# Performance work log

Hardware: AMD Instinct MI355X
Metric: run time of the kernel (lower is better)

Reference implementation:

```python
import jax, jax.numpy as jnp
import numpy as np

ROI = 7
NMS_THR = 0.01
NMS_SIZE = 100


def crop_and_resize(fmap, boxes, crop):
    # fmap [H,W,C], boxes [N,4] normalized (y1,x1,y2,x2) -> [N,crop,crop,C]
    H, W, C = fmap.shape
    t = jnp.linspace(0.0, 1.0, crop)
    ys = (boxes[:, 0:1] + (boxes[:, 2:3] - boxes[:, 0:1]) * t) * (H - 1)  # [N,crop]
    xs = (boxes[:, 1:2] + (boxes[:, 3:4] - boxes[:, 1:2]) * t) * (W - 1)
    y0 = jnp.clip(jnp.floor(ys), 0, H - 1).astype(jnp.int32)
    x0 = jnp.clip(jnp.floor(xs), 0, W - 1).astype(jnp.int32)
    y1 = jnp.clip(y0 + 1, 0, H - 1)
    x1 = jnp.clip(x0 + 1, 0, W - 1)
    wy = (ys - y0)[:, :, None, None]
    wx = (xs - x0)[:, None, :, None]
    Y0, Y1 = y0[:, :, None], y1[:, :, None]
    X0, X1 = x0[:, None, :], x1[:, None, :]
    f00 = fmap[Y0, X0]; f01 = fmap[Y0, X1]
    f10 = fmap[Y1, X0]; f11 = fmap[Y1, X1]
    return (f00 * (1 - wy) * (1 - wx) + f01 * (1 - wy) * wx
            + f10 * wy * (1 - wx) + f11 * wy * wx)


def iou_matrix(b):
    # b [N,4] (x1,y1,x2,y2)
    area = jnp.maximum(b[:, 2] - b[:, 0], 0) * jnp.maximum(b[:, 3] - b[:, 1], 0)
    lt = jnp.maximum(b[:, None, :2], b[None, :, :2])
    rb = jnp.minimum(b[:, None, 2:], b[None, :, 2:])
    wh = jnp.maximum(rb - lt, 0.0)
    inter = wh[..., 0] * wh[..., 1]
    return inter / (area[:, None] + area[None, :] - inter + 1e-8)


def nms(boxes, scores, thr, max_out):
    # greedy NMS, fixed-size output (pads with lowest-ranked boxes when fewer survive)
    N = boxes.shape[0]
    order = jnp.argsort(-scores)
    M = iou_matrix(boxes[order])
    idx = jnp.arange(N)
    def body(i, keep):
        sup = (M[i] > thr) & (idx > i) & keep[i]
        return keep & ~sup
    keep = jax.lax.fori_loop(0, N, body, jnp.ones(N, dtype=bool))
    rank = jnp.where(keep, idx, N + idx)
    sel = jnp.argsort(rank)[:max_out]
    return order[sel]


def make_boxes(key, n):
    kc, ks = jax.random.split(key)
    c = jax.random.uniform(kc, (n, 2), minval=0.1, maxval=0.9)
    s = jax.random.uniform(ks, (n, 2), minval=0.02, maxval=0.15)
    lo = jnp.clip(c - s / 2, 0.0, 1.0)
    hi = jnp.clip(c + s / 2, 0.0, 1.0)
    return jnp.concatenate([lo, hi], axis=1)  # (y1,x1,y2,x2)


def setup_inputs() -> dict:
    key = jax.random.key(0)
    ks = jax.random.split(key, 12)
    N, D, Hd = 1024, ROI * ROI * 32, 2048
    img_boxes = make_boxes(ks[0], N)
    bev_boxes = make_boxes(ks[1], N)
    bev_boxes_abs = bev_boxes[:, jnp.array([1, 0, 3, 2])] * 80.0  # (x1,y1,x2,y2) in meters
    def w(k, shape, fan_in):
        return jax.random.normal(k, shape, jnp.float32) * (2.0 / fan_in) ** 0.5
    return {
        'img_feat_map': jax.random.uniform(ks[2], (1, 360, 1200, 32), jnp.float32),
        'bev_feat_map': jax.random.uniform(ks[3], (1, 700, 800, 32), jnp.float32),
        'img_boxes': img_boxes,
        'bev_boxes': bev_boxes,
        'bev_boxes_abs': bev_boxes_abs,
        'img_mask': jnp.ones((1, 1, 1, 1), jnp.float32),
        'bev_mask': jnp.ones((1, 1, 1, 1), jnp.float32),
        'W1': w(ks[4], (D, Hd), D), 'b1': jnp.zeros((Hd,), jnp.float32),
        'W2': w(ks[5], (Hd, Hd), Hd), 'b2': jnp.zeros((Hd,), jnp.float32),
        'Wc': w(ks[6], (Hd, 2), Hd), 'bc': jnp.zeros((2,), jnp.float32),
        'Wo': w(ks[7], (Hd, 10), Hd), 'bo': jnp.zeros((10,), jnp.float32),
        'Wa': w(ks[8], (Hd, 2), Hd), 'ba': jnp.zeros((2,), jnp.float32),
    }


def reference(img_feat_map, bev_feat_map, img_boxes, bev_boxes, bev_boxes_abs,
              img_mask, bev_mask, W1, b1, W2, b2, Wc, bc, Wo, bo, Wa, ba):
    # ROI align on masked feature maps
    rois_rgb = crop_and_resize((img_mask * img_feat_map)[0], img_boxes, ROI)
    rois_bev = crop_and_resize((bev_mask * bev_feat_map)[0], bev_boxes, ROI)
    # mean fusion
    fused = (rois_rgb + rois_bev) / (img_mask + bev_mask)  # [N,7,7,32]
    # predictor
    x = fused.reshape(fused.shape[0], -1)
    h = jax.nn.relu(x @ W1 + b1)
    h = jax.nn.relu(h @ W2 + b2)
    obj = h @ Wc + bc            # [N,2]
    off = h @ Wo + bo            # [N,10]
    ang = h @ Wa + ba            # [N,2]
    obj_soft = jax.nn.softmax(obj, axis=1)
    orient = jnp.arctan2(ang[:, 1], ang[:, 0])  # convert_angle_to_orientation
    # offset-adjusted BEV boxes for NMS
    pb = bev_boxes_abs + 0.1 * off[:, :4]
    boxes = jnp.stack([jnp.minimum(pb[:, 0], pb[:, 2]), jnp.minimum(pb[:, 1], pb[:, 3]),
                       jnp.maximum(pb[:, 0], pb[:, 2]), jnp.maximum(pb[:, 1], pb[:, 3])], axis=1)
    scores = jnp.max(obj[:, 1:], axis=1)
    ti = nms(jax.lax.stop_gradient(boxes), jax.lax.stop_gradient(scores), NMS_THR, NMS_SIZE)
    # [100, 2 + 4 + 1]: softmax scores, pred bev boxes, orientations
    return jnp.concatenate([obj_soft[ti], boxes[ti], orient[ti][:, None]], axis=1)
```

## Files before the change

kernel.cpp:

```cpp
#include <hip/hip_runtime.h>
#include <math.h>

#define NBOX 1024
#define ROI_N 7
#define CH 32
#define FEAT (ROI_N*ROI_N*CH)
#define K1PAD 1664
#define HD 2048
#define NMS_THR_F 0.01f
#define NMS_OUT 100
#define MTRI_WORDS 8704

typedef _Float16 f16;
typedef f16 f16x4 __attribute__((ext_vector_type(4)));
typedef f16 f16x8 __attribute__((ext_vector_type(8)));
typedef float f32x4 __attribute__((ext_vector_type(4)));

__device__ __forceinline__ void split_f16(float v, f16& h, f16& l) {
  h = (f16)v;
  l = (f16)((v - (float)h) * 4096.0f);
}

__device__ __forceinline__ void gload_lds16(const void* g, void* l) {
  __builtin_amdgcn_global_load_lds(
      (const __attribute__((address_space(1))) unsigned int*)g,
      (__attribute__((address_space(3))) unsigned int*)l, 16, 0, 0);
}

#define B_ROI 1024
#define B_C1  (64*26)
#define B_C2  (64*32)
#define B_INIT 2048

__device__ void roi_part(int b, int tid,
    const float* __restrict__ img, const float* __restrict__ bev,
    const float* __restrict__ img_boxes, const float* __restrict__ bev_boxes,
    float mi, float mb, f16* __restrict__ xh, f16* __restrict__ xl)
{
  const float denom = mi + mb;
  if (tid >= 196) {
    const int g = tid - 196;
    if (g < 12) {
      f16x8 z = {};
      *(f16x8*)&xh[(size_t)b*K1PAD + FEAT + g*8] = z;
      *(f16x8*)&xl[(size_t)b*K1PAD + FEAT + g*8] = z;
    }
    return;
  }
  const int cell = tid >> 2, cg = (tid & 3) * 8;
  const int ti = cell / ROI_N, tj = cell - ti*ROI_N;
  const float tt_i = (ti == 6) ? 1.0f : ti * (1.0f/6.0f);
  const float tt_j = (tj == 6) ? 1.0f : tj * (1.0f/6.0f);

  float vi[8], vb[8];
  {
    const int H = 360, W = 1200;
    const float iy0 = img_boxes[b*4+0], ix0 = img_boxes[b*4+1];
    const float iy1 = img_boxes[b*4+2], ix1 = img_boxes[b*4+3];
    const float ys = (iy0 + (iy1 - iy0) * tt_i) * (float)(H-1);
    const float xs = (ix0 + (ix1 - ix0) * tt_j) * (float)(W-1);
    int y0 = (int)floorf(ys); y0 = y0 < 0 ? 0 : (y0 > H-1 ? H-1 : y0);
    int x0 = (int)floorf(xs); x0 = x0 < 0 ? 0 : (x0 > W-1 ? W-1 : x0);
    const int y1 = (y0+1 > H-1) ? H-1 : y0+1;
    const int x1 = (x0+1 > W-1) ? W-1 : x0+1;
    const float wy = ys - (float)y0, wx = xs - (float)x0;
    const float w00 = (1.0f-wy)*(1.0f-wx), w01 = (1.0f-wy)*wx;
    const float w10 = wy*(1.0f-wx),        w11 = wy*wx;
    const float* p00 = &img[(y0*W + x0)*CH + cg];
    const float* p01 = &img[(y0*W + x1)*CH + cg];
    const float* p10 = &img[(y1*W + x0)*CH + cg];
    const float* p11 = &img[(y1*W + x1)*CH + cg];
#pragma unroll
    for (int q = 0; q < 2; ++q) {
      const float4 f00 = *(const float4*)(p00 + q*4);
      const float4 f01 = *(const float4*)(p01 + q*4);
      const float4 f10 = *(const float4*)(p10 + q*4);
      const float4 f11 = *(const float4*)(p11 + q*4);
      vi[q*4+0] = f00.x*w00 + f01.x*w01 + f10.x*w10 + f11.x*w11;
      vi[q*4+1] = f00.y*w00 + f01.y*w01 + f10.y*w10 + f11.y*w11;
      vi[q*4+2] = f00.z*w00 + f01.z*w01 + f10.z*w10 + f11.z*w11;
      vi[q*4+3] = f00.w*w00 + f01.w*w01 + f10.w*w10 + f11.w*w11;
    }
  }
  {
    const int H = 700, W = 800;
    const float by0 = bev_boxes[b*4+0], bx0 = bev_boxes[b*4+1];
    const float by1 = bev_boxes[b*4+2], bx1 = bev_boxes[b*4+3];
    const float ys = (by0 + (by1 - by0) * tt_i) * (float)(H-1);
    const float xs = (bx0 + (bx1 - bx0) * tt_j) * (float)(W-1);
    int y0 = (int)floorf(ys); y0 = y0 < 0 ? 0 : (y0 > H-1 ? H-1 : y0);
    int x0 = (int)floorf(xs); x0 = x0 < 0 ? 0 : (x0 > W-1 ? W-1 : x0);
    const int y1 = (y0+1 > H-1) ? H-1 : y0+1;
    const int x1 = (x0+1 > W-1) ? W-1 : x0+1;
    const float wy = ys - (float)y0, wx = xs - (float)x0;
    const float w00 = (1.0f-wy)*(1.0f-wx), w01 = (1.0f-wy)*wx;
    const float w10 = wy*(1.0f-wx),        w11 = wy*wx;
    const float* p00 = &bev[(y0*W + x0)*CH + cg];
    const float* p01 = &bev[(y0*W + x1)*CH + cg];
    const float* p10 = &bev[(y1*W + x0)*CH + cg];
    const float* p11 = &bev[(y1*W + x1)*CH + cg];
#pragma unroll
    for (int q = 0; q < 2; ++q) {
      const float4 f00 = *(const float4*)(p00 + q*4);
      const float4 f01 = *(const float4*)(p01 + q*4);
      const float4 f10 = *(const float4*)(p10 + q*4);
      const float4 f11 = *(const float4*)(p11 + q*4);
      vb[q*4+0] = f00.x*w00 + f01.x*w01 + f10.x*w10 + f11.x*w11;
      vb[q*4+1] = f00.y*w00 + f01.y*w01 + f10.y*w10 + f11.y*w11;
      vb[q*4+2] = f00.z*w00 + f01.z*w01 + f10.z*w10 + f11.z*w11;
      vb[q*4+3] = f00.w*w00 + f01.w*w01 + f10.w*w10 + f11.w*w11;
    }
  }
  f16x8 h8, l8;
#pragma unroll
  for (int q = 0; q < 8; ++q) {
    f16 h, l;
    split_f16((mi*vi[q] + mb*vb[q]) / denom, h, l);
    h8[q] = h; l8[q] = l;
  }
  const size_t o = (size_t)b*K1PAD + cell*32 + cg;
  *(f16x8*)&xh[o] = h8;
  *(f16x8*)&xl[o] = l8;
}

__global__ __launch_bounds__(256) void prep_kernel(
    const float* __restrict__ img, const float* __restrict__ bev,
    const float* __restrict__ img_boxes, const float* __restrict__ bev_boxes,
    const float* __restrict__ img_mask, const float* __restrict__ bev_mask,
    f16* __restrict__ xh, f16* __restrict__ xl,
    const float* __restrict__ W1, f16* __restrict__ Wt1h, f16* __restrict__ Wt1l,
    const float* __restrict__ W2, f16* __restrict__ Wt2h, f16* __restrict__ Wt2l,
    const float* __restrict__ b1, const float* __restrict__ b2,
    float4* __restrict__ h1f, float4* __restrict__ h2f)
{
  __shared__ float t[64][33];
  const int g = blockIdx.x;
  const int tid = threadIdx.x;

  if (g < B_ROI) {
    roi_part(g, tid, img, bev, img_boxes, bev_boxes, img_mask[0], bev_mask[0], xh, xl);
    return;
  }
  const float* W; f16 *Wh, *Wl; int K, Kpad, cb;
  if (g < B_ROI + B_C1) { cb = g - B_ROI;        W = W1; Wh = Wt1h; Wl = Wt1l; K = FEAT; Kpad = K1PAD; }
  else if (g < B_ROI + B_C1 + B_C2) { cb = g - B_ROI - B_C1; W = W2; Wh = Wt2h; Wl = Wt2l; K = HD; Kpad = HD; }
  else {
    const int ib = g - B_ROI - B_C1 - B_C2;
    const int idx = ib*256 + tid;
    const int c4 = idx & (HD/4 - 1);
    h1f[idx] = *(const float4*)&b1[c4*4];
    h2f[idx] = *(const float4*)&b2[c4*4];
    return;
  }
  const int nt = cb & 63, kt = cb >> 6;
  const int n0 = nt * 32, k0 = kt * 64;
#pragma unroll
  for (int p = 0; p < 8; ++p) {
    const int idx = tid + p*256;
    const int kk = idx >> 5, nn = idx & 31;
    const int k = k0 + kk;
    t[kk][nn] = (k < K) ? W[(size_t)k*HD + n0 + nn] : 0.0f;
  }
  __syncthreads();
  const int nn = tid >> 3;
  const int kg = (tid & 7) * 8;
  f16x8 h8, l8;
#pragma unroll
  for (int q = 0; q < 8; ++q) {
    f16 h, l;
    split_f16(t[kg + q][nn], h, l);
    h8[q] = h; l8[q] = l;
  }
  *(f16x8*)&Wh[(size_t)(n0+nn)*Kpad + k0 + kg] = h8;
  *(f16x8*)&Wl[(size_t)(n0+nn)*Kpad + k0 + kg] = l8;
}

__global__ __launch_bounds__(256) void split_relu_kernel(
    const float* __restrict__ in, f16* __restrict__ oh, f16* __restrict__ ol)
{
  const int idx = blockIdx.x*256 + threadIdx.x;
  const float4 v = *(const float4*)&in[idx*4];
  f16x4 h4, l4;
  { f16 h,l; split_f16(fmaxf(v.x,0.0f),h,l); h4[0]=h; l4[0]=l; }
  { f16 h,l; split_f16(fmaxf(v.y,0.0f),h,l); h4[1]=h; l4[1]=l; }
  { f16 h,l; split_f16(fmaxf(v.z,0.0f),h,l); h4[2]=h; l4[2]=l; }
  { f16 h,l; split_f16(fmaxf(v.w,0.0f),h,l); h4[3]=h; l4[3]=l; }
  *(f16x4*)&oh[idx*4] = h4;
  *(f16x4*)&ol[idx*4] = l4;
}

__global__ __launch_bounds__(256, 2) void gemm_sk(
    const f16* __restrict__ Ah_g, const f16* __restrict__ Al_g,
    const f16* __restrict__ Bh_g, const f16* __restrict__ Bl_g,
    float* __restrict__ Cout, int M, int N, int K, int kchunk)
{
  __shared__ __align__(16) f16 Ah[128][32], Al[128][32], Bh[128][32], Bl[128][32];
  const int tid = threadIdx.x;

  const int g = blockIdx.x;
  const int xcd = g & 7, c = g >> 3;
  const int nb = xcd*2 + (c & 1);
  const int mb = (c >> 1) & 7;
  const int zb = c >> 4;
  const int m0 = mb * 128, n0 = nb * 128;
  const int kb = zb * kchunk, ke = kb + kchunk;

  const int wid = tid >> 6, lane = tid & 63;
  const int wr = wid >> 1, wc = wid & 1;
  const int frow = lane & 15, fkg = lane >> 4;
  const int swz = (fkg ^ ((frow >> 1) & 3)) * 8;

  const f16* sarr; f16* larr; int rbase;
  if (wid == 0)      { sarr = Ah_g; larr = &Ah[0][0]; rbase = m0; }
  else if (wid == 1) { sarr = Al_g; larr = &Al[0][0]; rbase = m0; }
  else if (wid == 2) { sarr = Bh_g; larr = &Bh[0][0]; rbase = n0; }
  else               { sarr = Bl_g; larr = &Bl[0][0]; rbase = n0; }
  const int lr = lane >> 2, lg = lane & 3;

  f32x4 acc1[4][4], acc2[4][4];
#pragma unroll
  for (int i = 0; i < 4; ++i)
#pragma unroll
    for (int j = 0; j < 4; ++j)
#pragma unroll
      for (int r = 0; r < 4; ++r) { acc1[i][j][r] = 0.0f; acc2[i][j][r] = 0.0f; }

  for (int kk = kb; kk < ke; kk += 32) {
    __syncthreads();
#pragma unroll
    for (int q = 0; q < 8; ++q) {
      const int r = q*16 + lr;
      const int sg = lg ^ ((r >> 1) & 3);
      gload_lds16(&sarr[(size_t)(rbase + r)*K + kk + sg*8], larr + q*512);
    }
    __syncthreads();

    f16x8 bh[4], bl[4];
#pragma unroll
    for (int j = 0; j < 4; ++j) {
      const int rr = wc*64 + j*16 + frow;
      bh[j] = *(const f16x8*)&Bh[rr][swz];
      bl[j] = *(const f16x8*)&Bl[rr][swz];
    }
#pragma unroll
    for (int i = 0; i < 4; ++i) {
      const int rr = wr*64 + i*16 + frow;
      const f16x8 ah = *(const f16x8*)&Ah[rr][swz];
      const f16x8 al = *(const f16x8*)&Al[rr][swz];
#pragma unroll
      for (int j = 0; j < 4; ++j) {
        acc1[i][j] = __builtin_amdgcn_mfma_f32_16x16x32_f16(ah, bh[j], acc1[i][j], 0, 0, 0);
        acc2[i][j] = __builtin_amdgcn_mfma_f32_16x16x32_f16(ah, bl[j], acc2[i][j], 0, 0, 0);
        acc2[i][j] = __builtin_amdgcn_mfma_f32_16x16x32_f16(al, bh[j], acc2[i][j], 0, 0, 0);
      }
    }
  }

  const float s = 1.0f / 4096.0f;
#pragma unroll
  for (int i = 0; i < 4; ++i)
#pragma unroll
    for (int j = 0; j < 4; ++j) {
      const int col = n0 + wc*64 + j*16 + frow;
#pragma unroll
      for (int r = 0; r < 4; ++r) {
        const int row = m0 + wr*64 + i*16 + fkg*4 + r;
        atomicAdd(&Cout[(size_t)row*N + col], acc1[i][j][r] + acc2[i][j][r] * s);
      }
    }
}

__global__ __launch_bounds__(256) void heads_kernel(
    const float* __restrict__ h2f,
    const float* __restrict__ Wc, const float* __restrict__ bc,
    const float* __restrict__ Wo, const float* __restrict__ bo,
    const float* __restrict__ Wa, const float* __restrict__ ba,
    const float* __restrict__ bev_abs,
    float* __restrict__ obj_soft, float* __restrict__ boxes,
    float* __restrict__ orient, float* __restrict__ scores)
{
  const int r = blockIdx.x;
  const int tid = threadIdx.x;
  float acc[14];
#pragma unroll
  for (int j = 0; j < 14; ++j) acc[j] = 0.0f;
  for (int k = tid; k < HD; k += 256) {
    const float hv = fmaxf(h2f[(size_t)r*HD + k], 0.0f);
    acc[0]  += hv * Wc[k*2+0];
    acc[1]  += hv * Wc[k*2+1];
#pragma unroll
    for (int j = 0; j < 10; ++j) acc[2+j] += hv * Wo[k*10+j];
    acc[12] += hv * Wa[k*2+0];
    acc[13] += hv * Wa[k*2+1];
  }
  __shared__ float red[14][256];
#pragma unroll
  for (int j = 0; j < 14; ++j) red[j][tid] = acc[j];
  __syncthreads();
  for (int s = 128; s > 0; s >>= 1) {
    if (tid < s) {
#pragma unroll
      for (int j = 0; j < 14; ++j) red[j][tid] += red[j][tid + s];
    }
    __syncthreads();
  }
  if (tid == 0) {
    const float obj0 = red[0][0] + bc[0];
    const float obj1 = red[1][0] + bc[1];
    float off0 = red[2][0] + bo[0];
    float off1 = red[3][0] + bo[1];
    float off2 = red[4][0] + bo[2];
    float off3 = red[5][0] + bo[3];
    const float a0 = red[12][0] + ba[0];
    const float a1 = red[13][0] + ba[1];

    const float m  = fmaxf(obj0, obj1);
    const float e0 = expf(obj0 - m), e1 = expf(obj1 - m);
    const float se = e0 + e1;
    obj_soft[r*2+0] = e0 / se;
    obj_soft[r*2+1] = e1 / se;
    orient[r] = atan2f(a1, a0);

    const float pb0 = bev_abs[r*4+0] + 0.1f*off0;
    const float pb1 = bev_abs[r*4+1] + 0.1f*off1;
    const float pb2 = bev_abs[r*4+2] + 0.1f*off2;
    const float pb3 = bev_abs[r*4+3] + 0.1f*off3;
    boxes[r*4+0] = fminf(pb0, pb2);
    boxes[r*4+1] = fminf(pb1, pb3);
    boxes[r*4+2] = fmaxf(pb0, pb2);
    boxes[r*4+3] = fmaxf(pb1, pb3);
    scores[r] = obj1;
  }
}

__global__ __launch_bounds__(128) void sort_kernel(
    const float* __restrict__ scores, const float* __restrict__ boxes,
    int* __restrict__ order, float4* __restrict__ sboxes, float* __restrict__ sarea)
{
  const int i = blockIdx.x * 128 + threadIdx.x;
  const float my = scores[i];
  int pos = 0;
  for (int j = 0; j < NBOX; ++j) {
    const float sj = scores[j];
    pos += (sj > my) || (sj == my && j < i);
  }
  const float b0 = boxes[i*4+0], b1 = boxes[i*4+1];
  const float b2 = boxes[i*4+2], b3 = boxes[i*4+3];
  order[pos]  = i;
  sboxes[pos] = make_float4(b0, b1, b2, b3);
  sarea[pos]  = fmaxf(b2 - b0, 0.0f) * fmaxf(b3 - b1, 0.0f);
}

__device__ __forceinline__ int tri_base(int i) {
  const int b = i >> 6;
  return 64*(16*b - (b*(b-1))/2) + (i & 63)*(16 - b);
}

__global__ __launch_bounds__(256) void maskbuild_kernel(
    const float4* __restrict__ sboxes, const float* __restrict__ sarea,
    unsigned long long* __restrict__ Mtri)
{
  __shared__ float4 sb[NBOX];
  __shared__ float  sa[NBOX];
  const int tid = threadIdx.x;
  for (int t = tid; t < NBOX; t += 256) { sb[t] = sboxes[t]; sa[t] = sarea[t]; }
  __syncthreads();
  const int wv = tid >> 6, lane = tid & 63;
  for (int r = 0; r < 4; ++r) {
    const int i = blockIdx.x * 16 + wv * 4 + r;
    const float4 bi = sb[i];
    const float  ai = sa[i];
    const int b = i >> 6;
    const int base = tri_base(i);
    for (int w = b; w < 16; ++w) {
      const int j = w * 64 + lane;
      const float4 bj = sb[j];
      const float lt0 = fmaxf(bi.x, bj.x), lt1 = fmaxf(bi.y, bj.y);
      const float rb0 = fminf(bi.z, bj.z), rb1 = fminf(bi.w, bj.w);
      const float wq = fmaxf(rb0 - lt0, 0.0f), hq = fmaxf(rb1 - lt1, 0.0f);
      const float inter = wq * hq;
      const float iou = inter / (ai + sa[j] - inter + 1e-8f);
      const unsigned long long bits = __ballot((j > i) && (iou > NMS_THR_F));
      if (lane == 0) Mtri[base + (w - b)] = bits;
    }
  }
}

__global__ __launch_bounds__(1024) void scan_out_kernel(
    const unsigned long long* __restrict__ Mtri_g, const int* __restrict__ order,
    const float4* __restrict__ sboxes, const float* __restrict__ obj_soft,
    const float* __restrict__ orient, float* __restrict__ out)
{
  __shared__ unsigned long long M[MTRI_WORDS];
  __shared__ unsigned long long keepw[16];
  const int tid = threadIdx.x;
  for (int t = tid; t < MTRI_WORDS; t += 1024) M[t] = Mtri_g[t];
  __syncthreads();

  if (tid < 64) {
    const int lane = tid;
    unsigned long long kw = (lane < 16) ? ~0ull : 0ull;
    for (int w = 0; w < 16; ++w) {
      unsigned long long rem = __shfl(kw, w);
      while (rem) {
        const int bpos = __builtin_ctzll(rem);
        const int i = w * 64 + bpos;
        const int base = tri_base(i);
        unsigned long long m = 0;
        if (lane >= w && lane < 16) m = M[base + (lane - w)];
        kw &= ~m;
        const unsigned long long updated = __shfl(kw, w);
        rem = (bpos == 63) ? 0ull : (updated & (~0ull << (bpos + 1)));
      }
    }
    if (lane < 16) keepw[lane] = kw;
  }
  __syncthreads();

  const int w = tid >> 6, bpos = tid & 63;
  int pre = 0, total = 0;
#pragma unroll
  for (int q = 0; q < 16; ++q) {
    const int pc = __popcll(keepw[q]);
    total += pc;
    if (q < w) pre += pc;
  }
  pre += __popcll(keepw[w] & ((bpos == 0) ? 0ull : (~0ull >> (64 - bpos))));
  const int keep_self = (int)((keepw[w] >> bpos) & 1ull);
  const int rank = keep_self ? pre : (total + tid - pre);

  if (rank < NMS_OUT) {
    const int ob = order[tid];
    const float4 bx = sboxes[tid];
    out[rank*7+0] = obj_soft[ob*2+0];
    out[rank*7+1] = obj_soft[ob*2+1];
    out[rank*7+2] = bx.x;
    out[rank*7+3] = bx.y;
    out[rank*7+4] = bx.z;
    out[rank*7+5] = bx.w;
    out[rank*7+6] = orient[ob];
  }
}

extern "C" void kernel_launch(void* const* d_in, const int* in_sizes, int n_in,
                              void* d_out, int out_size, void* d_ws, size_t ws_size,
                              hipStream_t stream) {
  (void)in_sizes; (void)n_in; (void)out_size; (void)ws_size;
  const float* img       = (const float*)d_in[0];
  const float* bev       = (const float*)d_in[1];
  const float* img_boxes = (const float*)d_in[2];
  const float* bev_boxes = (const float*)d_in[3];
  const float* bev_abs   = (const float*)d_in[4];
  const float* img_mask  = (const float*)d_in[5];
  const float* bev_mask  = (const float*)d_in[6];
  const float* W1 = (const float*)d_in[7];
  const float* b1 = (const float*)d_in[8];
  const float* W2 = (const float*)d_in[9];
  const float* b2 = (const float*)d_in[10];
  const float* Wc = (const float*)d_in[11];
  const float* bc = (const float*)d_in[12];
  const float* Wo = (const float*)d_in[13];
  const float* bo = (const float*)d_in[14];
  const float* Wa = (const float*)d_in[15];
  const float* ba = (const float*)d_in[16];
  float* out = (float*)d_out;

  char* ws = (char*)d_ws;
  f16* xh    = (f16*)ws;                                  ws += (size_t)NBOX*K1PAD*2;
  f16* xl    = (f16*)ws;                                  ws += (size_t)NBOX*K1PAD*2;
  float* h1f = (float*)ws;                                ws += (size_t)NBOX*HD*4;
  f16* h1h   = (f16*)ws;                                  ws += (size_t)NBOX*HD*2;
  f16* h1l   = (f16*)ws;                                  ws += (size_t)NBOX*HD*2;
  float* h2f = (float*)ws;                                ws += (size_t)NBOX*HD*4;
  f16* Wt1h  = (f16*)ws;                                  ws += (size_t)HD*K1PAD*2;
  f16* Wt1l  = (f16*)ws;                                  ws += (size_t)HD*K1PAD*2;
  f16* Wt2h  = (f16*)ws;                                  ws += (size_t)HD*HD*2;
  f16* Wt2l  = (f16*)ws;                                  ws += (size_t)HD*HD*2;
  float* obj_soft = (float*)ws;                           ws += NBOX*2*4;
  float* boxesf   = (float*)ws;                           ws += NBOX*4*4;
  float* orient   = (float*)ws;                           ws += NBOX*4;
  float* scores   = (float*)ws;                           ws += NBOX*4;
  int*   order    = (int*)ws;                             ws += NBOX*4;
  float4* sboxes  = (float4*)ws;                          ws += NBOX*16;
  float* sarea    = (float*)ws;                           ws += NBOX*4;
  unsigned long long* Mtri = (unsigned long long*)ws;

  prep_kernel<<<B_ROI + B_C1 + B_C2 + B_INIT, 256, 0, stream>>>(
      img, bev, img_boxes, bev_boxes, img_mask, bev_mask, xh, xl,
      W1, Wt1h, Wt1l, W2, Wt2h, Wt2l, b1, b2, (float4*)h1f, (float4*)h2f);
  gemm_sk<<<512, 256, 0, stream>>>(xh, xl, Wt1h, Wt1l, h1f, NBOX, HD, K1PAD, K1PAD/4);
  split_relu_kernel<<<NBOX*HD/4/256, 256, 0, stream>>>(h1f, h1h, h1l);
  gemm_sk<<<512, 256, 0, stream>>>(h1h, h1l, Wt2h, Wt2l, h2f, NBOX, HD, HD, HD/4);
  heads_kernel<<<NBOX, 256, 0, stream>>>(h2f, Wc, bc, Wo, bo, Wa, ba, bev_abs,
                                         obj_soft, boxesf, orient, scores);
  sort_kernel<<<8, 128, 0, stream>>>(scores, boxesf, order, sboxes, sarea);
  maskbuild_kernel<<<64, 256, 0, stream>>>(sboxes, sarea, Mtri);
  scan_out_kernel<<<1, 1024, 0, stream>>>(Mtri, order, sboxes, obj_soft, orient, out);
}
```

Before: 359.2 us.

## Double-buffer GEMM LDS staging, transpose head weights, cache scores in LDS

The split-K GEMM now uses two LDS buffers and issues the global-to-LDS loads for the next K step before computing on the current one, so there is one barrier per iteration instead of two. The head weights are concatenated and transposed into a contiguous [14][HD] array in the prep kernel, which lets the heads kernel read hidden values and weights as vectorized float4 loads. The sort kernel first copies the scores into shared memory. Doubling LDS use to 64KB per block may lower occupancy below the two blocks the launch bounds request.

Result: faster. 345.3 us (-3.9%).

```diff
diff --git a/kernel.cpp b/kernel.cpp
--- a/kernel.cpp
+++ b/kernel.cpp
@@ -31,6 +31,7 @@
 #define B_C1  (64*26)
 #define B_C2  (64*32)
 #define B_INIT 2048
+#define B_HT  112
 
 __device__ void roi_part(int b, int tid,
     const float* __restrict__ img, const float* __restrict__ bev,
@@ -131,7 +132,9 @@
     const float* __restrict__ W1, f16* __restrict__ Wt1h, f16* __restrict__ Wt1l,
     const float* __restrict__ W2, f16* __restrict__ Wt2h, f16* __restrict__ Wt2l,
     const float* __restrict__ b1, const float* __restrict__ b2,
-    float4* __restrict__ h1f, float4* __restrict__ h2f)
+    float4* __restrict__ h1f, float4* __restrict__ h2f,
+    const float* __restrict__ Wc, const float* __restrict__ Wo,
+    const float* __restrict__ Wa, float* __restrict__ Wcat)
 {
   __shared__ float t[64][33];
   const int g = blockIdx.x;
@@ -139,6 +142,16 @@
 
   if (g < B_ROI) {
     roi_part(g, tid, img, bev, img_boxes, bev_boxes, img_mask[0], bev_mask[0], xh, xl);
+    return;
+  }
+  if (g >= B_ROI + B_C1 + B_C2 + B_INIT) {
+    const int idx = (g - (B_ROI + B_C1 + B_C2 + B_INIT))*256 + tid;
+    const int j = idx >> 11, k = idx & (HD-1);
+    float v;
+    if (j < 2)       v = Wc[k*2 + j];
+    else if (j < 12) v = Wo[k*10 + (j-2)];
+    else             v = Wa[k*2 + (j-12)];
+    Wcat[idx] = v;
     return;
   }
   const float* W; f16 *Wh, *Wl; int K, Kpad, cb;
@@ -189,12 +202,23 @@
   *(f16x4*)&ol[idx*4] = l4;
 }
 
+#define STAGE(BUF, KK)                                                        \
+  do {                                                                        \
+    _Pragma("unroll")                                                         \
+    for (int q_ = 0; q_ < 8; ++q_) {                                          \
+      const int r_ = q_*16 + lr;                                              \
+      const int sg_ = lg ^ ((r_ >> 1) & 3);                                   \
+      gload_lds16(&sarr[(size_t)(rbase + r_)*K + (KK) + sg_*8],               \
+                  lbase + (BUF)*16384 + q_*512);                              \
+    }                                                                         \
+  } while (0)
+
 __global__ __launch_bounds__(256, 2) void gemm_sk(
     const f16* __restrict__ Ah_g, const f16* __restrict__ Al_g,
     const f16* __restrict__ Bh_g, const f16* __restrict__ Bl_g,
     float* __restrict__ Cout, int M, int N, int K, int kchunk)
 {
-  __shared__ __align__(16) f16 Ah[128][32], Al[128][32], Bh[128][32], Bl[128][32];
+  __shared__ __align__(16) f16 lds[2][4][128*32];
   const int tid = threadIdx.x;
 
   const int g = blockIdx.x;
@@ -210,11 +234,12 @@
   const int frow = lane & 15, fkg = lane >> 4;
   const int swz = (fkg ^ ((frow >> 1) & 3)) * 8;
 
-  const f16* sarr; f16* larr; int rbase;
-  if (wid == 0)      { sarr = Ah_g; larr = &Ah[0][0]; rbase = m0; }
-  else if (wid == 1) { sarr = Al_g; larr = &Al[0][0]; rbase = m0; }
-  else if (wid == 2) { sarr = Bh_g; larr = &Bh[0][0]; rbase = n0; }
-  else               { sarr = Bl_g; larr = &Bl[0][0]; rbase = n0; }
+  const f16* sarr; int rbase;
+  if (wid == 0)      { sarr = Ah_g; rbase = m0; }
+  else if (wid == 1) { sarr = Al_g; rbase = m0; }
+  else if (wid == 2) { sarr = Bh_g; rbase = n0; }
+  else               { sarr = Bl_g; rbase = n0; }
+  f16* lbase = &lds[0][wid][0];
   const int lr = lane >> 2, lg = lane & 3;
 
   f32x4 acc1[4][4], acc2[4][4];
@@ -225,28 +250,25 @@
 #pragma unroll
       for (int r = 0; r < 4; ++r) { acc1[i][j][r] = 0.0f; acc2[i][j][r] = 0.0f; }
 
+  STAGE(0, kb);
+  __syncthreads();
+  int cur = 0;
   for (int kk = kb; kk < ke; kk += 32) {
-    __syncthreads();
-#pragma unroll
-    for (int q = 0; q < 8; ++q) {
-      const int r = q*16 + lr;
-      const int sg = lg ^ ((r >> 1) & 3);
-      gload_lds16(&sarr[(size_t)(rbase + r)*K + kk + sg*8], larr + q*512);
-    }
-    __syncthreads();
-
+    if (kk + 32 < ke) STAGE(cur ^ 1, kk + 32);
+
+    const f16* bc_ = &lds[cur][0][0];
     f16x8 bh[4], bl[4];
 #pragma unroll
     for (int j = 0; j < 4; ++j) {
       const int rr = wc*64 + j*16 + frow;
-      bh[j] = *(const f16x8*)&Bh[rr][swz];
-      bl[j] = *(const f16x8*)&Bl[rr][swz];
+      bh[j] = *(const f16x8*)(bc_ + 8192  + rr*32 + swz);
+      bl[j] = *(const f16x8*)(bc_ + 12288 + rr*32 + swz);
     }
 #pragma unroll
     for (int i = 0; i < 4; ++i) {
       const int rr = wr*64 + i*16 + frow;
-      const f16x8 ah = *(const f16x8*)&Ah[rr][swz];
-      const f16x8 al = *(const f16x8*)&Al[rr][swz];
+      const f16x8 ah = *(const f16x8*)(bc_ +        rr*32 + swz);
+      const f16x8 al = *(const f16x8*)(bc_ + 4096 + rr*32 + swz);
 #pragma unroll
       for (int j = 0; j < 4; ++j) {
         acc1[i][j] = __builtin_amdgcn_mfma_f32_16x16x32_f16(ah, bh[j], acc1[i][j], 0, 0, 0);
@@ -254,6 +276,8 @@
         acc2[i][j] = __builtin_amdgcn_mfma_f32_16x16x32_f16(al, bh[j], acc2[i][j], 0, 0, 0);
       }
     }
+    __syncthreads();
+    cur ^= 1;
   }
 
   const float s = 1.0f / 4096.0f;
@@ -271,27 +295,29 @@
 }
 
 __global__ __launch_bounds__(256) void heads_kernel(
-    const float* __restrict__ h2f,
-    const float* __restrict__ Wc, const float* __restrict__ bc,
-    const float* __restrict__ Wo, const float* __restrict__ bo,
-    const float* __restrict__ Wa, const float* __restrict__ ba,
-    const float* __restrict__ bev_abs,
+    const float* __restrict__ h2f, const float* __restrict__ Wcat,
+    const float* __restrict__ bc, const float* __restrict__ bo,
+    const float* __restrict__ ba, const float* __restrict__ bev_abs,
     float* __restrict__ obj_soft, float* __restrict__ boxes,
     float* __restrict__ orient, float* __restrict__ scores)
 {
   const int r = blockIdx.x;
   const int tid = threadIdx.x;
+  const int k0 = tid * 8;
+  float4 hv0 = *(const float4*)&h2f[(size_t)r*HD + k0];
+  float4 hv1 = *(const float4*)&h2f[(size_t)r*HD + k0 + 4];
+  hv0.x = fmaxf(hv0.x, 0.0f); hv0.y = fmaxf(hv0.y, 0.0f);
+  hv0.z = fmaxf(hv0.z, 0.0f); hv0.w = fmaxf(hv0.w, 0.0f);
+  hv1.x = fmaxf(hv1.x, 0.0f); hv1.y = fmaxf(hv1.y, 0.0f);
+  hv1.z = fmaxf(hv1.z, 0.0f); hv1.w = fmaxf(hv1.w, 0.0f);
+
   float acc[14];
 #pragma unroll
-  for (int j = 0; j < 14; ++j) acc[j] = 0.0f;
-  for (int k = tid; k < HD; k += 256) {
-    const float hv = fmaxf(h2f[(size_t)r*HD + k], 0.0f);
-    acc[0]  += hv * Wc[k*2+0];
-    acc[1]  += hv * Wc[k*2+1];
-#pragma unroll
-    for (int j = 0; j < 10; ++j) acc[2+j] += hv * Wo[k*10+j];
-    acc[12] += hv * Wa[k*2+0];
-    acc[13] += hv * Wa[k*2+1];
+  for (int j = 0; j < 14; ++j) {
+    const float4 w0 = *(const float4*)&Wcat[j*HD + k0];
+    const float4 w1 = *(const float4*)&Wcat[j*HD + k0 + 4];
+    acc[j] = hv0.x*w0.x + hv0.y*w0.y + hv0.z*w0.z + hv0.w*w0.w
+           + hv1.x*w1.x + hv1.y*w1.y + hv1.z*w1.z + hv1.w*w1.w;
   }
   __shared__ float red[14][256];
 #pragma unroll
@@ -307,10 +333,10 @@
   if (tid == 0) {
     const float obj0 = red[0][0] + bc[0];
     const float obj1 = red[1][0] + bc[1];
-    float off0 = red[2][0] + bo[0];
-    float off1 = red[3][0] + bo[1];
-    float off2 = red[4][0] + bo[2];
-    float off3 = red[5][0] + bo[3];
+    const float off0 = red[2][0] + bo[0];
+    const float off1 = red[3][0] + bo[1];
+    const float off2 = red[4][0] + bo[2];
+    const float off3 = red[5][0] + bo[3];
     const float a0 = red[12][0] + ba[0];
     const float a1 = red[13][0] + ba[1];
 
@@ -337,11 +363,15 @@
     const float* __restrict__ scores, const float* __restrict__ boxes,
     int* __restrict__ order, float4* __restrict__ sboxes, float* __restrict__ sarea)
 {
-  const int i = blockIdx.x * 128 + threadIdx.x;
-  const float my = scores[i];
+  __shared__ float ss[NBOX];
+  const int tid = threadIdx.x;
+  for (int t = tid; t < NBOX; t += 128) ss[t] = scores[t];
+  __syncthreads();
+  const int i = blockIdx.x * 128 + tid;
+  const float my = ss[i];
   int pos = 0;
   for (int j = 0; j < NBOX; ++j) {
-    const float sj = scores[j];
+    const float sj = ss[j];
     pos += (sj > my) || (sj == my && j < i);
   }
   const float b0 = boxes[i*4+0], b1 = boxes[i*4+1];
@@ -476,6 +506,7 @@
   f16* Wt1l  = (f16*)ws;                                  ws += (size_t)HD*K1PAD*2;
   f16* Wt2h  = (f16*)ws;                                  ws += (size_t)HD*HD*2;
   f16* Wt2l  = (f16*)ws;                                  ws += (size_t)HD*HD*2;
+  float* Wcat = (float*)ws;                               ws += 14*HD*4;
   float* obj_soft = (float*)ws;                           ws += NBOX*2*4;
   float* boxesf   = (float*)ws;                           ws += NBOX*4*4;
   float* orient   = (float*)ws;                           ws += NBOX*4;
@@ -485,13 +516,14 @@
   float* sarea    = (float*)ws;                           ws += NBOX*4;
   unsigned long long* Mtri = (unsigned long long*)ws;
 
-  prep_kernel<<<B_ROI + B_C1 + B_C2 + B_INIT, 256, 0, stream>>>(
+  prep_kernel<<<B_ROI + B_C1 + B_C2 + B_INIT + B_HT, 256, 0, stream>>>(
       img, bev, img_boxes, bev_boxes, img_mask, bev_mask, xh, xl,
-      W1, Wt1h, Wt1l, W2, Wt2h, Wt2l, b1, b2, (float4*)h1f, (float4*)h2f);
+      W1, Wt1h, Wt1l, W2, Wt2h, Wt2l, b1, b2, (float4*)h1f, (float4*)h2f,
+      Wc, Wo, Wa, Wcat);
   gemm_sk<<<512, 256, 0, stream>>>(xh, xl, Wt1h, Wt1l, h1f, NBOX, HD, K1PAD, K1PAD/4);
   split_relu_kernel<<<NBOX*HD/4/256, 256, 0, stream>>>(h1f, h1h, h1l);
   gemm_sk<<<512, 256, 0, stream>>>(h1h, h1l, Wt2h, Wt2l, h2f, NBOX, HD, HD, HD/4);
-  heads_kernel<<<NBOX, 256, 0, stream>>>(h2f, Wc, bc, Wo, bo, Wa, ba, bev_abs,
+  heads_kernel<<<NBOX, 256, 0, stream>>>(h2f, Wcat, bc, bo, ba, bev_abs,
                                          obj_soft, boxesf, orient, scores);
   sort_kernel<<<8, 128, 0, stream>>>(scores, boxesf, order, sboxes, sarea);
   maskbuild_kernel<<<64, 256, 0, stream>>>(sboxes, sarea, Mtri);
```
